# Kernel optimization log

Measured on AMD Instinct MI355X. Metric: run time of the kernel, lower is better.

Reference implementation:

```python
import jax, jax.numpy as jnp
import numpy as np

R = 4          # num_roles
L = 2          # num_layers
DIN = 128      # input/hidden feature dim
DOUT = 40     # output classes
N = 40000      # nodes
E = 480000     # edges


def setup_inputs() -> dict:
    key = jax.random.key(0)
    ks = jax.random.split(key, 12)
    x = jax.random.normal(ks[0], (N, R + DIN), dtype=jnp.float32)
    edge_index = jax.random.randint(ks[1], (2, E), 0, N, dtype=jnp.int64)
    s = 0.05
    Wm = jax.random.normal(ks[2], (L, R, DIN, DIN), dtype=jnp.float32) * s
    bm = jax.random.normal(ks[3], (L, R, DIN), dtype=jnp.float32) * s
    Wa = jax.random.normal(ks[4], (L, R, 2 * DIN, DIN), dtype=jnp.float32) * s
    ba = jax.random.normal(ks[5], (L, R, DIN), dtype=jnp.float32) * s
    W1 = jax.random.normal(ks[6], (DIN, DIN), dtype=jnp.float32) * s
    b1 = jax.random.normal(ks[7], (DIN,), dtype=jnp.float32) * s
    W2 = jax.random.normal(ks[8], (DIN, DOUT), dtype=jnp.float32) * s
    b2 = jax.random.normal(ks[9], (DOUT,), dtype=jnp.float32) * s
    return {"x": x, "edge_index": edge_index, "Wm": Wm, "bm": bm,
            "Wa": Wa, "ba": ba, "W1": W1, "b1": b1, "W2": W2, "b2": b2}


def _role_coef(roles):
    # Faithful to the original loop bug: linears[0] applied twice with roles[:,0],
    # linears[r] with roles[:,r] for r=1..R-2, linears[R-1] unused.
    return jnp.concatenate(
        [2.0 * roles[:, :1], roles[:, 1:R - 1], jnp.zeros_like(roles[:, :1])], axis=1)


def _graphsage_layer(xfull, src, dst, Wm_l, bm_l, Wa_l, ba_l):
    roles = xfull[:, :R]          # [N, R]
    feats = xfull[:, R:]          # [N, D]
    # --- message: gather source nodes, per-role linear + weighted sum, relu ---
    xr = roles[src]               # [E, R]
    xf = feats[src]               # [E, D]
    coef = _role_coef(xr)         # [E, R]
    lin = jnp.einsum('ei,rio->ero', xf, Wm_l) + bm_l[None]   # [E, R, O]
    msg = jax.nn.relu(jnp.einsum('er,ero->eo', coef, lin))    # [E, O]
    # --- aggregate: scatter-mean to target nodes ---
    ssum = jax.ops.segment_sum(msg, dst, num_segments=N)      # [N, O]
    cnt = jax.ops.segment_sum(jnp.ones((msg.shape[0], 1), msg.dtype), dst,
                              num_segments=N)                 # [N, 1]
    aggr = jnp.where(cnt > 0, ssum / jnp.maximum(cnt, 1.0), 0.0)
    # --- update: concat, per-role linear + weighted sum, relu, L2 normalize ---
    cat = jnp.concatenate([feats, aggr], axis=1)              # [N, D+O]
    coefn = _role_coef(roles)                                 # [N, R]
    lin2 = jnp.einsum('ni,rio->nro', cat, Wa_l) + ba_l[None]  # [N, R, O]
    out = jax.nn.relu(jnp.einsum('nr,nro->no', coefn, lin2))  # [N, O]
    norm = jnp.linalg.norm(out, axis=1, keepdims=True)
    return out / jnp.maximum(norm, 1e-12)


def reference(x, edge_index, Wm, bm, Wa, ba, W1, b1, W2, b2):
    src = edge_index[0]
    dst = edge_index[1]
    h = x
    for l in range(L):
        feats = _graphsage_layer(h, src, dst, Wm[l], bm[l], Wa[l], ba[l])
        feats = jax.nn.relu(feats)  # extra relu from GNNStack (dropout is identity in eval)
        h = jnp.concatenate([h[:, :R], feats], axis=1)
    z = h[:, R:]
    z = z @ W1 + b1               # post_mp linear 1 (dropout identity)
    logits = z @ W2 + b2          # post_mp linear 2
    return jax.nn.log_softmax(logits, axis=1)
```

## Files before the change

### kernel.cpp

```cpp
#include <hip/hip_runtime.h>
#include <hip/hip_fp16.h>

#define RN 4
#define XSTRIDE 132

typedef float    frag_cd __attribute__((ext_vector_type(4)));
typedef _Float16 frag_h  __attribute__((ext_vector_type(8)));

#define CW_M  (6 * 128 * 128)
#define CW_A  (6 * 128 * 256)
#define CW_1  (128 * 128)
#define CW_2  (48 * 128)
#define CW_TOT (CW_M + CW_A + CW_1 + CW_2)

__global__ void prep_kernel(
    const float* __restrict__ Wm, const float* __restrict__ Wa,
    const float* __restrict__ W1, const float* __restrict__ W2,
    _Float16* __restrict__ WmT, _Float16* __restrict__ WaT,
    _Float16* __restrict__ W1T, _Float16* __restrict__ W2T,
    const float* __restrict__ x, _Float16* __restrict__ X,
    const int* __restrict__ ei, int* __restrict__ cnt, int N, int E)
{
    int id = blockIdx.x * 256 + threadIdx.x;
    if (id < CW_M) {
        const int K = 128;
        int per = K * 128;
        int lr = id / per;  int l = lr / 3, r = lr - l * 3;
        int rem = id - lr * per;
        int k = rem >> 7, col = rem & 127;
        WmT[((size_t)lr * 128 + col) * K + k] =
            (_Float16)Wm[(((size_t)l * 4 + r) * K + k) * 128 + col];
        return;
    }
    id -= CW_M;
    if (id < CW_A) {
        const int K = 256;
        int per = K * 128;
        int lr = id / per;  int l = lr / 3, r = lr - l * 3;
        int rem = id - lr * per;
        int k = rem >> 7, col = rem & 127;
        WaT[((size_t)lr * 128 + col) * K + k] =
            (_Float16)Wa[(((size_t)l * 4 + r) * K + k) * 128 + col];
        return;
    }
    id -= CW_A;
    if (id < CW_1) {
        int col = id >> 7, k = id & 127;
        W1T[id] = (_Float16)W1[k * 128 + col];
        return;
    }
    id -= CW_1;
    if (id < CW_2) {
        int col = id >> 7, k = id & 127;
        W2T[id] = (_Float16)((col < 40) ? W2[k * 40 + col] : 0.0f);
        return;
    }
    id -= CW_2;
    if (id < N * 16) {
        int n = id >> 4, g = id & 15;
        const float4* src = (const float4*)(x + (size_t)n * XSTRIDE + RN + g * 8);
        float4 f0 = src[0], f1 = src[1];
        __half2 h0 = __float22half2_rn(make_float2(f0.x, f0.y));
        __half2 h1 = __float22half2_rn(make_float2(f0.z, f0.w));
        __half2 h2 = __float22half2_rn(make_float2(f1.x, f1.y));
        __half2 h3 = __float22half2_rn(make_float2(f1.z, f1.w));
        uint4 st; st.x = *(uint*)&h0; st.y = *(uint*)&h1;
        st.z = *(uint*)&h2; st.w = *(uint*)&h3;
        ((uint4*)X)[(size_t)n * 16 + g] = st;
        return;
    }
    id -= N * 16;
    if (id < E) atomicAdd(&cnt[ei[E + id]], 1);
}

__global__ void scanA(const int* __restrict__ cnt, int N, int* __restrict__ bsums) {
    __shared__ int s[256];
    int t = threadIdx.x, n = blockIdx.x * 256 + t;
    s[t] = (n < N) ? cnt[n] : 0;
    __syncthreads();
    for (int off = 128; off > 0; off >>= 1) {
        if (t < off) s[t] += s[t + off];
        __syncthreads();
    }
    if (t == 0) bsums[blockIdx.x] = s[0];
}

__global__ void scanC(const int* __restrict__ cnt, int N, int nb,
                      const int* __restrict__ bsums, int* __restrict__ offs) {
    __shared__ int s[256];
    __shared__ int basebuf[256];
    int t = threadIdx.x, n = blockIdx.x * 256 + t;
    int bid = blockIdx.x;
    basebuf[t] = (t < bid && t < nb) ? bsums[t] : 0;
    __syncthreads();
    for (int off = 128; off > 0; off >>= 1) {
        if (t < off) basebuf[t] += basebuf[t + off];
        __syncthreads();
    }
    int base = basebuf[0];
    int v = (n < N) ? cnt[n] : 0;
    s[t] = v; __syncthreads();
    for (int off = 1; off < 256; off <<= 1) {
        int add = (t >= off) ? s[t - off] : 0;
        __syncthreads();
        s[t] += add;
        __syncthreads();
    }
    if (n < N) {
        offs[n] = base + s[t] - v;
        if (n == N - 1) offs[N] = base + s[t];
    }
}

__global__ void fill_kernel(const int* __restrict__ ei, int E,
                            const int* __restrict__ offs, int* __restrict__ fc,
                            int* __restrict__ csr) {
    int e = blockIdx.x * 256 + threadIdx.x;
    if (e < E) {
        int dst = ei[E + e];
        int p = offs[dst] + atomicAdd(&fc[dst], 1);
        csr[p] = ei[e];
    }
}

__global__ __launch_bounds__(256) void agg_kernel(
    const int* __restrict__ csr, const int* __restrict__ offs,
    const _Float16* __restrict__ Mb, _Float16* __restrict__ S, int N)
{
    int node = blockIdx.x * 16 + (threadIdx.x >> 4);
    int lane = threadIdx.x & 15;
    if (node >= N) return;
    int lo = offs[node], hi = offs[node + 1];
    const uint4* M4 = (const uint4*)Mb;
    float a[8];
    #pragma unroll
    for (int i = 0; i < 8; ++i) a[i] = 0.0f;
    int e = lo;
    for (; e + 3 < hi; e += 4) {
        #pragma unroll
        for (int j = 0; j < 4; ++j) {
            uint4 u = M4[(size_t)csr[e + j] * 16 + lane];
            float2 f0 = __half22float2(*(const __half2*)&u.x);
            float2 f1 = __half22float2(*(const __half2*)&u.y);
            float2 f2 = __half22float2(*(const __half2*)&u.z);
            float2 f3 = __half22float2(*(const __half2*)&u.w);
            a[0] += f0.x; a[1] += f0.y; a[2] += f1.x; a[3] += f1.y;
            a[4] += f2.x; a[5] += f2.y; a[6] += f3.x; a[7] += f3.y;
        }
    }
    for (; e < hi; ++e) {
        uint4 u = M4[(size_t)csr[e] * 16 + lane];
        float2 f0 = __half22float2(*(const __half2*)&u.x);
        float2 f1 = __half22float2(*(const __half2*)&u.y);
        float2 f2 = __half22float2(*(const __half2*)&u.z);
        float2 f3 = __half22float2(*(const __half2*)&u.w);
        a[0] += f0.x; a[1] += f0.y; a[2] += f1.x; a[3] += f1.y;
        a[4] += f2.x; a[5] += f2.y; a[6] += f3.x; a[7] += f3.y;
    }
    float inv = (hi > lo) ? 1.0f / (float)(hi - lo) : 0.0f;
    __half2 h0 = __float22half2_rn(make_float2(a[0] * inv, a[1] * inv));
    __half2 h1 = __float22half2_rn(make_float2(a[2] * inv, a[3] * inv));
    __half2 h2 = __float22half2_rn(make_float2(a[4] * inv, a[5] * inv));
    __half2 h3 = __float22half2_rn(make_float2(a[6] * inv, a[7] * inv));
    uint4 st; st.x = *(uint*)&h0; st.y = *(uint*)&h1;
    st.z = *(uint*)&h2; st.w = *(uint*)&h3;
    ((uint4*)S)[(size_t)node * 16 + lane] = st;
}

template<int KV, bool NORM>
__global__ __launch_bounds__(256) void gemm_mfma(
    const float* __restrict__ x,
    const _Float16* __restrict__ Fp,
    const _Float16* __restrict__ Sp,
    const _Float16* __restrict__ W,
    const float* __restrict__ bias,
    _Float16* __restrict__ out)
{
    __shared__ float cc[64][3];
    __shared__ float red[64][4];

    const int tid = threadIdx.x;
    const int n0 = blockIdx.x * 64;
    const int lane = tid & 63;
    const int wv = tid >> 6;
    const int q = lane >> 4;
    const int lb = lane & 15;
    const int w32 = wv * 32;

    if (tid < 64) {
        const float* xr = x + (size_t)(n0 + tid) * XSTRIDE;
        cc[tid][0] = 2.0f * xr[0];
        cc[tid][1] = xr[1];
        cc[tid][2] = xr[2];
    }
    __syncthreads();

    _Float16 ch16[4][3];
    #pragma unroll
    for (int nt = 0; nt < 4; ++nt)
        #pragma unroll
        for (int r = 0; r < 3; ++r)
            ch16[nt][r] = (_Float16)cc[nt * 16 + lb][r];

    frag_cd acc[4][2];
    #pragma unroll
    for (int nt = 0; nt < 4; ++nt)
        #pragma unroll
        for (int ct = 0; ct < 2; ++ct)
            acc[nt][ct] = (frag_cd){0.f, 0.f, 0.f, 0.f};

    size_t wrow[3][2];
    #pragma unroll
    for (int r = 0; r < 3; ++r)
        #pragma unroll
        for (int ct = 0; ct < 2; ++ct)
            wrow[r][ct] = ((size_t)(r * 128 + w32 + ct * 16 + lb)) * KV + q * 8;

    size_t arow[4];
    #pragma unroll
    for (int nt = 0; nt < 4; ++nt)
        arow[nt] = (size_t)(n0 + nt * 16 + lb) * 128 + q * 8;

    if (KV == 128) {
        frag_h aF[4][4], bF[4][6];
        #pragma unroll
        for (int c = 0; c < 4; ++c) {
            #pragma unroll
            for (int nt = 0; nt < 4; ++nt)
                aF[c][nt] = *(const frag_h*)(Fp + arow[nt] + c * 32);
            #pragma unroll
            for (int r = 0; r < 3; ++r)
                #pragma unroll
                for (int ct = 0; ct < 2; ++ct)
                    bF[c][r * 2 + ct] = *(const frag_h*)(W + wrow[r][ct] + c * 32);
        }
        #pragma unroll
        for (int c = 0; c < 4; ++c)
            #pragma unroll
            for (int r = 0; r < 3; ++r)
                #pragma unroll
                for (int nt = 0; nt < 4; ++nt) {
                    frag_h sa = aF[c][nt] * ch16[nt][r];
                    #pragma unroll
                    for (int ct = 0; ct < 2; ++ct)
                        acc[nt][ct] = __builtin_amdgcn_mfma_f32_16x16x32_f16(
                            sa, bF[c][r * 2 + ct], acc[nt][ct], 0, 0, 0);
                }
    } else {
        const int NCH = KV / 32;
        frag_h aF[3][4], bF[3][6];
        auto loadChunk = [&](int c, int buf) {
            const _Float16* ap; int kofs;
            if (c < 4) { ap = Fp; kofs = c * 32; }
            else       { ap = Sp; kofs = (c - 4) * 32; }
            #pragma unroll
            for (int nt = 0; nt < 4; ++nt)
                aF[buf][nt] = *(const frag_h*)(ap + arow[nt] + kofs);
            #pragma unroll
            for (int r = 0; r < 3; ++r)
                #pragma unroll
                for (int ct = 0; ct < 2; ++ct)
                    bF[buf][r * 2 + ct] = *(const frag_h*)(W + wrow[r][ct] + c * 32);
        };
        loadChunk(0, 0);
        loadChunk(1, 1);
        #pragma unroll
        for (int ch = 0; ch < NCH; ++ch) {
            if (ch + 2 < NCH) loadChunk(ch + 2, (ch + 2) % 3);
            const int cur = ch % 3;
            #pragma unroll
            for (int r = 0; r < 3; ++r)
                #pragma unroll
                for (int nt = 0; nt < 4; ++nt) {
                    frag_h sa = aF[cur][nt] * ch16[nt][r];
                    #pragma unroll
                    for (int ct = 0; ct < 2; ++ct)
                        acc[nt][ct] = __builtin_amdgcn_mfma_f32_16x16x32_f16(
                            sa, bF[cur][r * 2 + ct], acc[nt][ct], 0, 0, 0);
                }
        }
    }

    float vv[4][2][4];
    #pragma unroll
    for (int ct = 0; ct < 2; ++ct) {
        int col = w32 + ct * 16 + lb;
        float b0 = bias[col], b1 = bias[128 + col], b2 = bias[256 + col];
        #pragma unroll
        for (int nt = 0; nt < 4; ++nt) {
            #pragma unroll
            for (int rg = 0; rg < 4; ++rg) {
                int row = nt * 16 + q * 4 + rg;
                float v = acc[nt][ct][rg]
                        + cc[row][0] * b0 + cc[row][1] * b1 + cc[row][2] * b2;
                vv[nt][ct][rg] = fmaxf(v, 0.0f);
            }
        }
    }

    if (NORM) {
        #pragma unroll
        for (int nt = 0; nt < 4; ++nt) {
            #pragma unroll
            for (int rg = 0; rg < 4; ++rg) {
                float ss = vv[nt][0][rg] * vv[nt][0][rg] + vv[nt][1][rg] * vv[nt][1][rg];
                #pragma unroll
                for (int m = 1; m < 16; m <<= 1) ss += __shfl_xor(ss, m, 64);
                if (lb == 0) red[nt * 16 + q * 4 + rg][wv] = ss;
            }
        }
        __syncthreads();
        #pragma unroll
        for (int nt = 0; nt < 4; ++nt) {
            #pragma unroll
            for (int rg = 0; rg < 4; ++rg) {
                int row = nt * 16 + q * 4 + rg;
                float t = red[row][0] + red[row][1] + red[row][2] + red[row][3];
                float inv = 1.0f / fmaxf(sqrtf(t), 1e-12f);
                #pragma unroll
                for (int ct = 0; ct < 2; ++ct) {
                    int col = w32 + ct * 16 + lb;
                    out[(size_t)(n0 + row) * 128 + col] = (_Float16)(vv[nt][ct][rg] * inv);
                }
            }
        }
    } else {
        #pragma unroll
        for (int nt = 0; nt < 4; ++nt)
            #pragma unroll
            for (int ct = 0; ct < 2; ++ct)
                #pragma unroll
                for (int rg = 0; rg < 4; ++rg) {
                    int row = nt * 16 + q * 4 + rg;
                    int col = w32 + ct * 16 + lb;
                    out[(size_t)(n0 + row) * 128 + col] = (_Float16)vv[nt][ct][rg];
                }
    }
}

__global__ __launch_bounds__(256) void final_mfma(
    const _Float16* __restrict__ F2,
    const _Float16* __restrict__ W1T,
    const float* __restrict__ b1,
    const _Float16* __restrict__ W2T,
    const float* __restrict__ b2,
    float* __restrict__ out)
{
    __shared__ _Float16 Z[64][136];

    const int tid = threadIdx.x;
    const int n0 = blockIdx.x * 64;
    const int lane = tid & 63;
    const int wv = tid >> 6;
    const int q = lane >> 4;
    const int lb = lane & 15;
    const int w32 = wv * 32;

    frag_cd acc[4][2];
    #pragma unroll
    for (int nt = 0; nt < 4; ++nt)
        #pragma unroll
        for (int ct = 0; ct < 2; ++ct) acc[nt][ct] = (frag_cd){0.f, 0.f, 0.f, 0.f};

    #pragma unroll
    for (int ch = 0; ch < 4; ++ch) {
        frag_h aF[4];
        #pragma unroll
        for (int nt = 0; nt < 4; ++nt)
            aF[nt] = *(const frag_h*)(F2 + (size_t)(n0 + nt * 16 + lb) * 128 + ch * 32 + q * 8);
        #pragma unroll
        for (int ct = 0; ct < 2; ++ct) {
            frag_h bF = *(const frag_h*)(W1T + (size_t)(w32 + ct * 16 + lb) * 128 + ch * 32 + q * 8);
            #pragma unroll
            for (int nt = 0; nt < 4; ++nt)
                acc[nt][ct] = __builtin_amdgcn_mfma_f32_16x16x32_f16(aF[nt], bF, acc[nt][ct], 0, 0, 0);
        }
    }
    #pragma unroll
    for (int ct = 0; ct < 2; ++ct) {
        int col = w32 + ct * 16 + lb;
        float bb = b1[col];
        #pragma unroll
        for (int nt = 0; nt < 4; ++nt)
            #pragma unroll
            for (int rg = 0; rg < 4; ++rg)
                Z[nt * 16 + q * 4 + rg][col] = (_Float16)(acc[nt][ct][rg] + bb);
    }
    __syncthreads();

    frag_cd a2[3];
    #pragma unroll
    for (int ct = 0; ct < 3; ++ct) a2[ct] = (frag_cd){0.f, 0.f, 0.f, 0.f};
    #pragma unroll
    for (int ch = 0; ch < 4; ++ch) {
        frag_h zF = *(const frag_h*)&Z[wv * 16 + lb][ch * 32 + q * 8];
        #pragma unroll
        for (int ct = 0; ct < 3; ++ct) {
            frag_h bF = *(const frag_h*)(W2T + (size_t)(ct * 16 + lb) * 128 + ch * 32 + q * 8);
            a2[ct] = __builtin_amdgcn_mfma_f32_16x16x32_f16(zF, bF, a2[ct], 0, 0, 0);
        }
    }

    float lg[3][4];
    #pragma unroll
    for (int ct = 0; ct < 3; ++ct) {
        int col = ct * 16 + lb;
        bool valid = col < 40;
        float bb = valid ? b2[col] : -1e30f;
        #pragma unroll
        for (int rg = 0; rg < 4; ++rg)
            lg[ct][rg] = valid ? (a2[ct][rg] + bb) : -1e30f;
    }
    #pragma unroll
    for (int rg = 0; rg < 4; ++rg) {
        float mx = fmaxf(fmaxf(lg[0][rg], lg[1][rg]), lg[2][rg]);
        #pragma unroll
        for (int m = 1; m < 16; m <<= 1) mx = fmaxf(mx, __shfl_xor(mx, m, 64));
        float sm = __expf(lg[0][rg] - mx) + __expf(lg[1][rg] - mx) + __expf(lg[2][rg] - mx);
        #pragma unroll
        for (int m = 1; m < 16; m <<= 1) sm += __shfl_xor(sm, m, 64);
        float ls = mx + __logf(sm);
        int row = n0 + wv * 16 + q * 4 + rg;
        #pragma unroll
        for (int ct = 0; ct < 3; ++ct) {
            int col = ct * 16 + lb;
            if (col < 40) out[(size_t)row * 40 + col] = lg[ct][rg] - ls;
        }
    }
}

extern "C" void kernel_launch(void* const* d_in, const int* in_sizes, int n_in,
                              void* d_out, int out_size, void* d_ws, size_t ws_size,
                              hipStream_t stream) {
    const float* x  = (const float*)d_in[0];
    const int*   ei = (const int*)d_in[1];
    const float* Wm = (const float*)d_in[2];
    const float* bm = (const float*)d_in[3];
    const float* Wa = (const float*)d_in[4];
    const float* ba = (const float*)d_in[5];
    const float* W1 = (const float*)d_in[6];
    const float* b1 = (const float*)d_in[7];
    const float* W2 = (const float*)d_in[8];
    const float* b2 = (const float*)d_in[9];
    float* out = (float*)d_out;

    const int N = in_sizes[0] / XSTRIDE;
    const int E = in_sizes[1] / 2;
    const int NB = (N + 255) / 256;
    const size_t P = (size_t)N * 128;

    _Float16* Mb  = (_Float16*)d_ws;
    _Float16* X   = Mb + P;
    _Float16* S   = X + P;
    _Float16* F1  = S + P;
    _Float16* WmT = F1 + P;
    _Float16* WaT = WmT + CW_M;
    _Float16* W1T = WaT + CW_A;
    _Float16* W2T = W1T + CW_1;
    int* cnt   = (int*)(W2T + CW_2);
    int* fc    = cnt + N;
    int* offs  = fc + N;
    int* csr   = offs + N + 1;
    int* bsums = csr + E;

    hipMemsetAsync(cnt, 0, (size_t)2 * N * sizeof(int), stream);
    const int prep_total = CW_TOT + N * 16 + E;
    prep_kernel<<<(prep_total + 255) / 256, 256, 0, stream>>>(
        Wm, Wa, W1, W2, WmT, WaT, W1T, W2T, x, X, ei, cnt, N, E);

    scanA<<<NB, 256, 0, stream>>>(cnt, N, bsums);
    scanC<<<NB, 256, 0, stream>>>(cnt, N, NB, bsums, offs);
    fill_kernel<<<(E + 255) / 256, 256, 0, stream>>>(ei, E, offs, fc, csr);

    const int gblk = N / 64;
    for (int l = 0; l < 2; ++l) {
        const _Float16* fp = (l == 0) ? X : F1;
        _Float16* o = (l == 0) ? F1 : X;

        gemm_mfma<128, false><<<gblk, 256, 0, stream>>>(
            x, fp, nullptr,
            WmT + (size_t)l * 3 * 128 * 128, bm + (size_t)l * 4 * 128, Mb);
        agg_kernel<<<(N + 15) / 16, 256, 0, stream>>>(csr, offs, Mb, S, N);
        gemm_mfma<256, true><<<gblk, 256, 0, stream>>>(
            x, fp, S,
            WaT + (size_t)l * 3 * 128 * 256, ba + (size_t)l * 4 * 128, o);
    }

    final_mfma<<<N / 64, 256, 0, stream>>>(X, W1T, b1, W2T, b2, out);
}
```

Before: 295.9 us.

## Fuse layer update with next message GEMM and with final MLP head

Layer-0 update GEMM now keeps its normalized output tile in shared memory and immediately computes the layer-1 message GEMM from it, writing both F1 and Mb. Layer-1 update is fused with the post-MP linear layers and log-softmax, so F2 never goes to global memory. This removes two kernel launches and the round trips of the intermediate feature tiles through HBM. In exchange it adds extra shared memory and register pressure per block, which may reduce occupancy.

```diff
diff --git a/kernel.cpp b/kernel.cpp
--- a/kernel.cpp
+++ b/kernel.cpp
@@ -167,17 +167,14 @@
     ((uint4*)S)[(size_t)node * 16 + lane] = st;
 }
 
-template<int KV, bool NORM>
-__global__ __launch_bounds__(256) void gemm_mfma(
+__global__ __launch_bounds__(256) void msg_kernel(
     const float* __restrict__ x,
     const _Float16* __restrict__ Fp,
-    const _Float16* __restrict__ Sp,
     const _Float16* __restrict__ W,
     const float* __restrict__ bias,
     _Float16* __restrict__ out)
 {
     __shared__ float cc[64][3];
-    __shared__ float red[64][4];
 
     const int tid = threadIdx.x;
     const int n0 = blockIdx.x * 64;
@@ -214,139 +211,158 @@
     for (int r = 0; r < 3; ++r)
         #pragma unroll
         for (int ct = 0; ct < 2; ++ct)
-            wrow[r][ct] = ((size_t)(r * 128 + w32 + ct * 16 + lb)) * KV + q * 8;
+            wrow[r][ct] = ((size_t)(r * 128 + w32 + ct * 16 + lb)) * 128 + q * 8;
 
     size_t arow[4];
     #pragma unroll
     for (int nt = 0; nt < 4; ++nt)
         arow[nt] = (size_t)(n0 + nt * 16 + lb) * 128 + q * 8;
 
-    if (KV == 128) {
-        frag_h aF[4][4], bF[4][6];
-        #pragma unroll
-        for (int c = 0; c < 4; ++c) {
-            #pragma unroll
-            for (int nt = 0; nt < 4; ++nt)
-                aF[c][nt] = *(const frag_h*)(Fp + arow[nt] + c * 32);
-            #pragma unroll
-            for (int r = 0; r < 3; ++r)
+    frag_h aF[4][4], bF[4][6];
+    #pragma unroll
+    for (int c = 0; c < 4; ++c) {
+        #pragma unroll
+        for (int nt = 0; nt < 4; ++nt)
+            aF[c][nt] = *(const frag_h*)(Fp + arow[nt] + c * 32);
+        #pragma unroll
+        for (int r = 0; r < 3; ++r)
+            #pragma unroll
+            for (int ct = 0; ct < 2; ++ct)
+                bF[c][r * 2 + ct] = *(const frag_h*)(W + wrow[r][ct] + c * 32);
+    }
+    #pragma unroll
+    for (int c = 0; c < 4; ++c)
+        #pragma unroll
+        for (int r = 0; r < 3; ++r)
+            #pragma unroll
+            for (int nt = 0; nt < 4; ++nt) {
+                frag_h sa = aF[c][nt] * ch16[nt][r];
                 #pragma unroll
                 for (int ct = 0; ct < 2; ++ct)
-                    bF[c][r * 2 + ct] = *(const frag_h*)(W + wrow[r][ct] + c * 32);
-        }
-        #pragma unroll
-        for (int c = 0; c < 4; ++c)
-            #pragma unroll
-            for (int r = 0; r < 3; ++r)
-                #pragma unroll
-                for (int nt = 0; nt < 4; ++nt) {
-                    frag_h sa = aF[c][nt] * ch16[nt][r];
-                    #pragma unroll
-                    for (int ct = 0; ct < 2; ++ct)
-                        acc[nt][ct] = __builtin_amdgcn_mfma_f32_16x16x32_f16(
-                            sa, bF[c][r * 2 + ct], acc[nt][ct], 0, 0, 0);
-                }
-    } else {
-        const int NCH = KV / 32;
-        frag_h aF[3][4], bF[3][6];
-        auto loadChunk = [&](int c, int buf) {
-            const _Float16* ap; int kofs;
-            if (c < 4) { ap = Fp; kofs = c * 32; }
-            else       { ap = Sp; kofs = (c - 4) * 32; }
-            #pragma unroll
-            for (int nt = 0; nt < 4; ++nt)
-                aF[buf][nt] = *(const frag_h*)(ap + arow[nt] + kofs);
-            #pragma unroll
-            for (int r = 0; r < 3; ++r)
-                #pragma unroll
-                for (int ct = 0; ct < 2; ++ct)
-                    bF[buf][r * 2 + ct] = *(const frag_h*)(W + wrow[r][ct] + c * 32);
-        };
-        loadChunk(0, 0);
-        loadChunk(1, 1);
-        #pragma unroll
-        for (int ch = 0; ch < NCH; ++ch) {
-            if (ch + 2 < NCH) loadChunk(ch + 2, (ch + 2) % 3);
-            const int cur = ch % 3;
-            #pragma unroll
-            for (int r = 0; r < 3; ++r)
-                #pragma unroll
-                for (int nt = 0; nt < 4; ++nt) {
-                    frag_h sa = aF[cur][nt] * ch16[nt][r];
-                    #pragma unroll
-                    for (int ct = 0; ct < 2; ++ct)
-                        acc[nt][ct] = __builtin_amdgcn_mfma_f32_16x16x32_f16(
-                            sa, bF[cur][r * 2 + ct], acc[nt][ct], 0, 0, 0);
-                }
-        }
-    }
-
-    float vv[4][2][4];
+                    acc[nt][ct] = __builtin_amdgcn_mfma_f32_16x16x32_f16(
+                        sa, bF[c][r * 2 + ct], acc[nt][ct], 0, 0, 0);
+            }
+
     #pragma unroll
     for (int ct = 0; ct < 2; ++ct) {
         int col = w32 + ct * 16 + lb;
         float b0 = bias[col], b1 = bias[128 + col], b2 = bias[256 + col];
         #pragma unroll
-        for (int nt = 0; nt < 4; ++nt) {
+        for (int nt = 0; nt < 4; ++nt)
             #pragma unroll
             for (int rg = 0; rg < 4; ++rg) {
                 int row = nt * 16 + q * 4 + rg;
                 float v = acc[nt][ct][rg]
                         + cc[row][0] * b0 + cc[row][1] * b1 + cc[row][2] * b2;
-                vv[nt][ct][rg] = fmaxf(v, 0.0f);
+                out[(size_t)(n0 + row) * 128 + col] = (_Float16)fmaxf(v, 0.0f);
             }
-        }
-    }
-
-    if (NORM) {
-        #pragma unroll
-        for (int nt = 0; nt < 4; ++nt) {
-            #pragma unroll
-            for (int rg = 0; rg < 4; ++rg) {
-                float ss = vv[nt][0][rg] * vv[nt][0][rg] + vv[nt][1][rg] * vv[nt][1][rg];
-                #pragma unroll
-                for (int m = 1; m < 16; m <<= 1) ss += __shfl_xor(ss, m, 64);
-                if (lb == 0) red[nt * 16 + q * 4 + rg][wv] = ss;
-            }
-        }
-        __syncthreads();
-        #pragma unroll
-        for (int nt = 0; nt < 4; ++nt) {
-            #pragma unroll
-            for (int rg = 0; rg < 4; ++rg) {
-                int row = nt * 16 + q * 4 + rg;
-                float t = red[row][0] + red[row][1] + red[row][2] + red[row][3];
-                float inv = 1.0f / fmaxf(sqrtf(t), 1e-12f);
-                #pragma unroll
-                for (int ct = 0; ct < 2; ++ct) {
-                    int col = w32 + ct * 16 + lb;
-                    out[(size_t)(n0 + row) * 128 + col] = (_Float16)(vv[nt][ct][rg] * inv);
-                }
-            }
-        }
-    } else {
-        #pragma unroll
-        for (int nt = 0; nt < 4; ++nt)
-            #pragma unroll
-            for (int ct = 0; ct < 2; ++ct)
-                #pragma unroll
-                for (int rg = 0; rg < 4; ++rg) {
-                    int row = nt * 16 + q * 4 + rg;
-                    int col = w32 + ct * 16 + lb;
-                    out[(size_t)(n0 + row) * 128 + col] = (_Float16)vv[nt][ct][rg];
-                }
-    }
-}
-
-__global__ __launch_bounds__(256) void final_mfma(
-    const _Float16* __restrict__ F2,
-    const _Float16* __restrict__ W1T,
-    const float* __restrict__ b1,
-    const _Float16* __restrict__ W2T,
-    const float* __restrict__ b2,
-    float* __restrict__ out)
+    }
+}
+
+#define UPDATE_PHASE_A(Fp, Sp, Wa_, ba_)                                      \
+    _Float16 ch16[4][3];                                                      \
+    _Pragma("unroll")                                                         \
+    for (int nt = 0; nt < 4; ++nt)                                            \
+        _Pragma("unroll")                                                     \
+        for (int r = 0; r < 3; ++r)                                           \
+            ch16[nt][r] = (_Float16)cc[nt * 16 + lb][r];                      \
+    frag_cd acc[4][2];                                                        \
+    _Pragma("unroll")                                                         \
+    for (int nt = 0; nt < 4; ++nt)                                            \
+        _Pragma("unroll")                                                     \
+        for (int ct = 0; ct < 2; ++ct)                                        \
+            acc[nt][ct] = (frag_cd){0.f, 0.f, 0.f, 0.f};                      \
+    size_t wrow[3][2];                                                        \
+    _Pragma("unroll")                                                         \
+    for (int r = 0; r < 3; ++r)                                               \
+        _Pragma("unroll")                                                     \
+        for (int ct = 0; ct < 2; ++ct)                                        \
+            wrow[r][ct] = ((size_t)(r * 128 + w32 + ct * 16 + lb)) * 256 + q * 8; \
+    size_t arow[4];                                                           \
+    _Pragma("unroll")                                                         \
+    for (int nt = 0; nt < 4; ++nt)                                            \
+        arow[nt] = (size_t)(n0 + nt * 16 + lb) * 128 + q * 8;                 \
+    {                                                                         \
+        frag_h aF[3][4], bF[3][6];                                            \
+        auto loadChunk = [&](int c, int buf) {                                \
+            const _Float16* ap; int kofs;                                     \
+            if (c < 4) { ap = (Fp); kofs = c * 32; }                          \
+            else       { ap = (Sp); kofs = (c - 4) * 32; }                    \
+            _Pragma("unroll")                                                 \
+            for (int nt = 0; nt < 4; ++nt)                                    \
+                aF[buf][nt] = *(const frag_h*)(ap + arow[nt] + kofs);         \
+            _Pragma("unroll")                                                 \
+            for (int r = 0; r < 3; ++r)                                       \
+                _Pragma("unroll")                                             \
+                for (int ct = 0; ct < 2; ++ct)                                \
+                    bF[buf][r * 2 + ct] = *(const frag_h*)((Wa_) + wrow[r][ct] + c * 32); \
+        };                                                                    \
+        loadChunk(0, 0);                                                      \
+        loadChunk(1, 1);                                                      \
+        _Pragma("unroll")                                                     \
+        for (int ch = 0; ch < 8; ++ch) {                                      \
+            if (ch + 2 < 8) loadChunk(ch + 2, (ch + 2) % 3);                  \
+            const int cur = ch % 3;                                           \
+            _Pragma("unroll")                                                 \
+            for (int r = 0; r < 3; ++r)                                       \
+                _Pragma("unroll")                                             \
+                for (int nt = 0; nt < 4; ++nt) {                              \
+                    frag_h sa = aF[cur][nt] * ch16[nt][r];                    \
+                    _Pragma("unroll")                                         \
+                    for (int ct = 0; ct < 2; ++ct)                            \
+                        acc[nt][ct] = __builtin_amdgcn_mfma_f32_16x16x32_f16( \
+                            sa, bF[cur][r * 2 + ct], acc[nt][ct], 0, 0, 0);   \
+                }                                                             \
+        }                                                                     \
+    }                                                                         \
+    float vv[4][2][4];                                                        \
+    _Pragma("unroll")                                                         \
+    for (int ct = 0; ct < 2; ++ct) {                                          \
+        int col = w32 + ct * 16 + lb;                                         \
+        float b0 = (ba_)[col], b1 = (ba_)[128 + col], b2 = (ba_)[256 + col];  \
+        _Pragma("unroll")                                                     \
+        for (int nt = 0; nt < 4; ++nt)                                        \
+            _Pragma("unroll")                                                 \
+            for (int rg = 0; rg < 4; ++rg) {                                  \
+                int row = nt * 16 + q * 4 + rg;                               \
+                float v = acc[nt][ct][rg]                                     \
+                        + cc[row][0] * b0 + cc[row][1] * b1 + cc[row][2] * b2;\
+                vv[nt][ct][rg] = fmaxf(v, 0.0f);                              \
+            }                                                                 \
+    }                                                                         \
+    _Pragma("unroll")                                                         \
+    for (int nt = 0; nt < 4; ++nt)                                            \
+        _Pragma("unroll")                                                     \
+        for (int rg = 0; rg < 4; ++rg) {                                      \
+            float ss = vv[nt][0][rg] * vv[nt][0][rg] + vv[nt][1][rg] * vv[nt][1][rg]; \
+            _Pragma("unroll")                                                 \
+            for (int m = 1; m < 16; m <<= 1) ss += __shfl_xor(ss, m, 64);     \
+            if (lb == 0) red[nt * 16 + q * 4 + rg][wv] = ss;                  \
+        }                                                                     \
+    __syncthreads();                                                          \
+    _Pragma("unroll")                                                         \
+    for (int nt = 0; nt < 4; ++nt)                                            \
+        _Pragma("unroll")                                                     \
+        for (int rg = 0; rg < 4; ++rg) {                                      \
+            int row = nt * 16 + q * 4 + rg;                                   \
+            float t = red[row][0] + red[row][1] + red[row][2] + red[row][3];  \
+            float inv = 1.0f / fmaxf(sqrtf(t), 1e-12f);                       \
+            _Pragma("unroll")                                                 \
+            for (int ct = 0; ct < 2; ++ct)                                    \
+                Fs[row][w32 + ct * 16 + lb] = (_Float16)(vv[nt][ct][rg] * inv); \
+        }                                                                     \
+    __syncthreads();
+
+__global__ __launch_bounds__(256) void fused_upd_msg(
+    const float* __restrict__ x,
+    const _Float16* __restrict__ Fp, const _Float16* __restrict__ Sp,
+    const _Float16* __restrict__ Wa_, const float* __restrict__ ba_,
+    const _Float16* __restrict__ Wm2, const float* __restrict__ bm2,
+    _Float16* __restrict__ F1, _Float16* __restrict__ Mb)
 {
-    __shared__ _Float16 Z[64][136];
+    __shared__ float cc[64][3];
+    __shared__ float red[64][4];
+    __shared__ _Float16 Fs[64][136];
 
     const int tid = threadIdx.x;
     const int n0 = blockIdx.x * 64;
@@ -356,25 +372,132 @@
     const int lb = lane & 15;
     const int w32 = wv * 32;
 
-    frag_cd acc[4][2];
+    if (tid < 64) {
+        const float* xr = x + (size_t)(n0 + tid) * XSTRIDE;
+        cc[tid][0] = 2.0f * xr[0];
+        cc[tid][1] = xr[1];
+        cc[tid][2] = xr[2];
+    }
+    __syncthreads();
+
+    UPDATE_PHASE_A(Fp, Sp, Wa_, ba_)
+
+    #pragma unroll
+    for (int i = 0; i < 4; ++i) {
+        int idx = i * 256 + tid;
+        int row = idx >> 4, g = idx & 15;
+        ((uint4*)F1)[(size_t)(n0 + row) * 16 + g] = *(const uint4*)&Fs[row][g * 8];
+    }
+
+    frag_cd a2[4][2];
     #pragma unroll
     for (int nt = 0; nt < 4; ++nt)
         #pragma unroll
-        for (int ct = 0; ct < 2; ++ct) acc[nt][ct] = (frag_cd){0.f, 0.f, 0.f, 0.f};
-
-    #pragma unroll
-    for (int ch = 0; ch < 4; ++ch) {
-        frag_h aF[4];
+        for (int ct = 0; ct < 2; ++ct)
+            a2[nt][ct] = (frag_cd){0.f, 0.f, 0.f, 0.f};
+
+    frag_h bB[4][6];
+    #pragma unroll
+    for (int c = 0; c < 4; ++c)
+        #pragma unroll
+        for (int r = 0; r < 3; ++r)
+            #pragma unroll
+            for (int ct = 0; ct < 2; ++ct)
+                bB[c][r * 2 + ct] = *(const frag_h*)(
+                    Wm2 + ((size_t)(r * 128 + w32 + ct * 16 + lb)) * 128 + c * 32 + q * 8);
+
+    #pragma unroll
+    for (int c = 0; c < 4; ++c) {
+        frag_h aM[4];
         #pragma unroll
         for (int nt = 0; nt < 4; ++nt)
-            aF[nt] = *(const frag_h*)(F2 + (size_t)(n0 + nt * 16 + lb) * 128 + ch * 32 + q * 8);
-        #pragma unroll
-        for (int ct = 0; ct < 2; ++ct) {
-            frag_h bF = *(const frag_h*)(W1T + (size_t)(w32 + ct * 16 + lb) * 128 + ch * 32 + q * 8);
+            aM[nt] = *(const frag_h*)&Fs[nt * 16 + lb][c * 32 + q * 8];
+        #pragma unroll
+        for (int r = 0; r < 3; ++r)
+            #pragma unroll
+            for (int nt = 0; nt < 4; ++nt) {
+                frag_h sa = aM[nt] * ch16[nt][r];
+                #pragma unroll
+                for (int ct = 0; ct < 2; ++ct)
+                    a2[nt][ct] = __builtin_amdgcn_mfma_f32_16x16x32_f16(
+                        sa, bB[c][r * 2 + ct], a2[nt][ct], 0, 0, 0);
+            }
+    }
+
+    #pragma unroll
+    for (int ct = 0; ct < 2; ++ct) {
+        int col = w32 + ct * 16 + lb;
+        float b0 = bm2[col], b1 = bm2[128 + col], b2 = bm2[256 + col];
+        #pragma unroll
+        for (int nt = 0; nt < 4; ++nt)
+            #pragma unroll
+            for (int rg = 0; rg < 4; ++rg) {
+                int row = nt * 16 + q * 4 + rg;
+                float v = a2[nt][ct][rg]
+                        + cc[row][0] * b0 + cc[row][1] * b1 + cc[row][2] * b2;
+                Mb[(size_t)(n0 + row) * 128 + col] = (_Float16)fmaxf(v, 0.0f);
+            }
+    }
+}
+
+__global__ __launch_bounds__(256) void fused_upd_final(
+    const float* __restrict__ x,
+    const _Float16* __restrict__ Fp, const _Float16* __restrict__ Sp,
+    const _Float16* __restrict__ Wa_, const float* __restrict__ ba_,
+    const _Float16* __restrict__ W1T, const float* __restrict__ b1,
+    const _Float16* __restrict__ W2T, const float* __restrict__ b2,
+    float* __restrict__ out)
+{
+    __shared__ float cc[64][3];
+    __shared__ float red[64][4];
+    __shared__ _Float16 Fs[64][136];
+    __shared__ _Float16 Z[64][136];
+
+    const int tid = threadIdx.x;
+    const int n0 = blockIdx.x * 64;
+    const int lane = tid & 63;
+    const int wv = tid >> 6;
+    const int q = lane >> 4;
+    const int lb = lane & 15;
+    const int w32 = wv * 32;
+
+    if (tid < 64) {
+        const float* xr = x + (size_t)(n0 + tid) * XSTRIDE;
+        cc[tid][0] = 2.0f * xr[0];
+        cc[tid][1] = xr[1];
+        cc[tid][2] = xr[2];
+    }
+    __syncthreads();
+
+    UPDATE_PHASE_A(Fp, Sp, Wa_, ba_)
+
+    frag_cd az[4][2];
+    #pragma unroll
+    for (int nt = 0; nt < 4; ++nt)
+        #pragma unroll
+        for (int ct = 0; ct < 2; ++ct)
+            az[nt][ct] = (frag_cd){0.f, 0.f, 0.f, 0.f};
+
+    frag_h bZ[4][2];
+    #pragma unroll
+    for (int c = 0; c < 4; ++c)
+        #pragma unroll
+        for (int ct = 0; ct < 2; ++ct)
+            bZ[c][ct] = *(const frag_h*)(
+                W1T + (size_t)(w32 + ct * 16 + lb) * 128 + c * 32 + q * 8);
+
+    #pragma unroll
+    for (int c = 0; c < 4; ++c) {
+        frag_h aZ[4];
+        #pragma unroll
+        for (int nt = 0; nt < 4; ++nt)
+            aZ[nt] = *(const frag_h*)&Fs[nt * 16 + lb][c * 32 + q * 8];
+        #pragma unroll
+        for (int ct = 0; ct < 2; ++ct)
             #pragma unroll
             for (int nt = 0; nt < 4; ++nt)
-                acc[nt][ct] = __builtin_amdgcn_mfma_f32_16x16x32_f16(aF[nt], bF, acc[nt][ct], 0, 0, 0);
-        }
+                az[nt][ct] = __builtin_amdgcn_mfma_f32_16x16x32_f16(
+                    aZ[nt], bZ[c][ct], az[nt][ct], 0, 0, 0);
     }
     #pragma unroll
     for (int ct = 0; ct < 2; ++ct) {
@@ -384,7 +507,7 @@
         for (int nt = 0; nt < 4; ++nt)
             #pragma unroll
             for (int rg = 0; rg < 4; ++rg)
-                Z[nt * 16 + q * 4 + rg][col] = (_Float16)(acc[nt][ct][rg] + bb);
+                Z[nt * 16 + q * 4 + rg][col] = (_Float16)(az[nt][ct][rg] + bb);
     }
     __syncthreads();
 
@@ -473,18 +596,15 @@
     fill_kernel<<<(E + 255) / 256, 256, 0, stream>>>(ei, E, offs, fc, csr);
 
     const int gblk = N / 64;
-    for (int l = 0; l < 2; ++l) {
-        const _Float16* fp = (l == 0) ? X : F1;
-        _Float16* o = (l == 0) ? F1 : X;
-
-        gemm_mfma<128, false><<<gblk, 256, 0, stream>>>(
-            x, fp, nullptr,
-            WmT + (size_t)l * 3 * 128 * 128, bm + (size_t)l * 4 * 128, Mb);
-        agg_kernel<<<(N + 15) / 16, 256, 0, stream>>>(csr, offs, Mb, S, N);
-        gemm_mfma<256, true><<<gblk, 256, 0, stream>>>(
-            x, fp, S,
-            WaT + (size_t)l * 3 * 128 * 256, ba + (size_t)l * 4 * 128, o);
-    }
-
-    final_mfma<<<N / 64, 256, 0, stream>>>(X, W1T, b1, W2T, b2, out);
-}
+    const int ablk = (N + 15) / 16;
+
+    msg_kernel<<<gblk, 256, 0, stream>>>(x, X, WmT, bm, Mb);
+    agg_kernel<<<ablk, 256, 0, stream>>>(csr, offs, Mb, S, N);
+    fused_upd_msg<<<gblk, 256, 0, stream>>>(
+        x, X, S, WaT, ba,
+        WmT + (size_t)3 * 128 * 128, bm + (size_t)4 * 128, F1, Mb);
+    agg_kernel<<<ablk, 256, 0, stream>>>(csr, offs, Mb, S, N);
+    fused_upd_final<<<gblk, 256, 0, stream>>>(
+        x, F1, S, WaT + (size_t)3 * 128 * 256, ba + (size_t)4 * 128,
+        W1T, b1, W2T, b2, out);
+}
```

Result: faster. 281.0 us (-5.0%).
